# Optimization experiments

Measured on AMD Instinct MI355X. Metric: run time of the kernel, lower is better.

The kernel has to match this reference:

```python
import jax, jax.numpy as jnp
import numpy as np

B, S, IN, H = 16, 512, 512, 256
TAU_TRACE = 20.0
TAU_MEM = 20.0
DECAY_TRACE = float(np.exp(-1.0 / TAU_TRACE))  # exp_convolve decay
DECAY_MEM = float(np.exp(-1.0 / TAU_MEM))      # leaky-integrator dynamics decay
LR = 0.01                                       # plasticity learning rate
W_MAX = 1.0                                     # soft upper bound on fast weights


def setup_inputs() -> dict:
    key = jax.random.key(0)
    k1, k2 = jax.random.split(key)
    x = jax.random.normal(k1, (B, S, IN), dtype=jnp.float32)
    # xavier_uniform with gain=sqrt(2) on W of shape [2H, IN]
    lim = float(np.sqrt(2.0) * np.sqrt(6.0 / (2 * H + IN)))
    W = jax.random.uniform(k2, (2 * H, IN), dtype=jnp.float32, minval=-lim, maxval=lim)
    return {"x": x, "W": W}


def reference(x, W):
    # i = x @ W^T : [B, S, 2H], then split into key/value input currents
    i = jnp.einsum('bsi,hi->bsh', x, W)
    ik, iv = jnp.split(i, 2, axis=2)  # each [B, S, H]
    bsz = x.shape[0]
    h = W.shape[0] // 2

    def step(carry, inp):
        kv, vv, kt, vt, mem = carry
        ik_t, iv_t = inp  # [B, H] each
        # key dynamics (leaky integrator + tanh)
        kv = DECAY_MEM * kv + ik_t
        key = jnp.tanh(kv)
        # memory readout: 0.2 * (key.unsqueeze(1) * mem).sum(2) == 0.2 * mem @ key
        ikv = 0.2 * jnp.einsum('bij,bj->bi', mem, key)
        # value dynamics
        vv = DECAY_MEM * vv + iv_t + ikv
        val = jnp.tanh(vv)
        # exponential traces
        kt = DECAY_TRACE * kt + (1.0 - DECAY_TRACE) * key
        vt = DECAY_TRACE * vt + (1.0 - DECAY_TRACE) * val
        # soft-bounded Hebbian outer-product fast-weight update
        mem = mem + LR * (vt[:, :, None] * kt[:, None, :]) * (W_MAX - mem)
        return (kv, vv, kt, vt, mem), (key, val)

    z = jnp.zeros((bsz, h), x.dtype)
    mem0 = jnp.zeros((bsz, h, h), x.dtype)
    (_, _, _, _, mem), (keys, vals) = jax.lax.scan(
        step, (z, z, z, z, mem0),
        (jnp.swapaxes(ik, 0, 1), jnp.swapaxes(iv, 0, 1)))  # scan over time
    return mem, jnp.swapaxes(keys, 0, 1), jnp.swapaxes(vals, 0, 1)
```

## Files before the change

### kernel.cpp

```cpp
#include <hip/hip_runtime.h>

#define BB 16
#define SS 512
#define KIN 512
#define H 256

typedef float v2f __attribute__((ext_vector_type(2)));

constexpr float DECAY  = 0.951229424500714f;
constexpr float OMD    = 0.048770575499286f;
constexpr float DECAY8 = 0.670320046035639f;
constexpr float LR     = 0.01f;
constexpr float CLO    = 4.8770575499286e-4f;

__device__ __forceinline__ float fast_tanh(float x) {
    float e = __expf(2.f * x);
    return 1.f - __fdividef(2.f, e + 1.f);
}

__device__ __forceinline__ v2f pk_mul(v2f a, v2f b) {
    v2f d; asm("v_pk_mul_f32 %0, %1, %2" : "=v"(d) : "v"(a), "v"(b)); return d;
}
__device__ __forceinline__ v2f pk_fma(v2f a, v2f b, v2f c) {
    v2f d; asm("v_pk_fma_f32 %0, %1, %2, %3" : "=v"(d) : "v"(a), "v"(b), "v"(c)); return d;
}

__device__ __forceinline__ void allred32x2(float x, float y, float& rx, float& ry) {
    int t, u;
    t = __builtin_amdgcn_update_dpp(0, __float_as_int(x), 0x111, 0xf, 0xf, false);
    u = __builtin_amdgcn_update_dpp(0, __float_as_int(y), 0x111, 0xf, 0xf, false);
    x += __int_as_float(t); y += __int_as_float(u);
    t = __builtin_amdgcn_update_dpp(0, __float_as_int(x), 0x112, 0xf, 0xf, false);
    u = __builtin_amdgcn_update_dpp(0, __float_as_int(y), 0x112, 0xf, 0xf, false);
    x += __int_as_float(t); y += __int_as_float(u);
    t = __builtin_amdgcn_update_dpp(0, __float_as_int(x), 0x114, 0xf, 0xf, false);
    u = __builtin_amdgcn_update_dpp(0, __float_as_int(y), 0x114, 0xf, 0xf, false);
    x += __int_as_float(t); y += __int_as_float(u);
    t = __builtin_amdgcn_update_dpp(0, __float_as_int(x), 0x118, 0xf, 0xf, false);
    u = __builtin_amdgcn_update_dpp(0, __float_as_int(y), 0x118, 0xf, 0xf, false);
    x += __int_as_float(t); y += __int_as_float(u);
    t = __builtin_amdgcn_update_dpp(0, __float_as_int(x), 0x142, 0xa, 0xf, false);
    u = __builtin_amdgcn_update_dpp(0, __float_as_int(y), 0x142, 0xa, 0xf, false);
    x += __int_as_float(t); y += __int_as_float(u);
    rx = __int_as_float(__builtin_amdgcn_ds_swizzle(__float_as_int(x), 0x3E0));
    ry = __int_as_float(__builtin_amdgcn_ds_swizzle(__float_as_int(y), 0x3E0));
}

__global__ __launch_bounds__(256) void gemm_xwT(const float* __restrict__ X,
                                                const float* __restrict__ W,
                                                float* __restrict__ ik_out,
                                                float* __restrict__ iv_t) {
    __shared__ float As[2][16][132];
    __shared__ float Bs[2][16][68];
    const int m0 = blockIdx.y * 128;
    const int n0 = blockIdx.x * 64;
    const int tid = threadIdx.x;
    const int ra = tid >> 1;
    const int ca = (tid & 1) * 8;
    const int rb = tid >> 2;
    const int cb = (tid & 3) * 4;
    const int tx = tid & 15;
    const int ty = tid >> 4;

    const float* xp = &X[(size_t)(m0 + ra) * KIN + ca];
    const float* wp = &W[(size_t)(n0 + rb) * KIN + cb];

    float acc[8][4] = {};
    float4 a0 = *(const float4*)(xp);
    float4 a1 = *(const float4*)(xp + 4);
    float4 bv = *(const float4*)(wp);
    As[0][ca+0][ra] = a0.x; As[0][ca+1][ra] = a0.y; As[0][ca+2][ra] = a0.z; As[0][ca+3][ra] = a0.w;
    As[0][ca+4][ra] = a1.x; As[0][ca+5][ra] = a1.y; As[0][ca+6][ra] = a1.z; As[0][ca+7][ra] = a1.w;
    Bs[0][cb+0][rb] = bv.x; Bs[0][cb+1][rb] = bv.y; Bs[0][cb+2][rb] = bv.z; Bs[0][cb+3][rb] = bv.w;
    __syncthreads();

    int cur = 0;
    for (int c = 0; c < KIN / 16; ++c) {
        if (c + 1 < KIN / 16) {
            a0 = *(const float4*)(xp + (size_t)(c + 1) * 16);
            a1 = *(const float4*)(xp + (size_t)(c + 1) * 16 + 4);
            bv = *(const float4*)(wp + (size_t)(c + 1) * 16);
        }
#pragma unroll
        for (int kk = 0; kk < 16; ++kk) {
            float4 A0 = *(const float4*)&As[cur][kk][ty * 8];
            float4 A1 = *(const float4*)&As[cur][kk][ty * 8 + 4];
            float4 B  = *(const float4*)&Bs[cur][kk][tx * 4];
            float arr[8] = {A0.x, A0.y, A0.z, A0.w, A1.x, A1.y, A1.z, A1.w};
            float brr[4] = {B.x, B.y, B.z, B.w};
#pragma unroll
            for (int i = 0; i < 8; ++i)
#pragma unroll
                for (int j = 0; j < 4; ++j) acc[i][j] += arr[i] * brr[j];
        }
        if (c + 1 < KIN / 16) {
            const int nb = cur ^ 1;
            As[nb][ca+0][ra] = a0.x; As[nb][ca+1][ra] = a0.y;
            As[nb][ca+2][ra] = a0.z; As[nb][ca+3][ra] = a0.w;
            As[nb][ca+4][ra] = a1.x; As[nb][ca+5][ra] = a1.y;
            As[nb][ca+6][ra] = a1.z; As[nb][ca+7][ra] = a1.w;
            Bs[nb][cb+0][rb] = bv.x; Bs[nb][cb+1][rb] = bv.y;
            Bs[nb][cb+2][rb] = bv.z; Bs[nb][cb+3][rb] = bv.w;
            __syncthreads();
            cur = nb;
        }
    }

    if (n0 < 256) {
#pragma unroll
        for (int i = 0; i < 8; ++i) {
            float4 o = make_float4(acc[i][0], acc[i][1], acc[i][2], acc[i][3]);
            *(float4*)&ik_out[(size_t)(m0 + ty * 8 + i) * 256 + n0 + tx * 4] = o;
        }
    } else {
        const int b  = m0 >> 9;
        const int s0 = (m0 & 511) + ty * 8;
#pragma unroll
        for (int j = 0; j < 4; ++j) {
            float* dst = &iv_t[((size_t)b * H + (n0 - 256 + tx * 4 + j)) * SS + s0];
            *(float4*)(dst)     = make_float4(acc[0][j], acc[1][j], acc[2][j], acc[3][j]);
            *(float4*)(dst + 4) = make_float4(acc[4][j], acc[5][j], acc[6][j], acc[7][j]);
        }
    }
}


__global__ __launch_bounds__(256) void ks1_chunk(const float* __restrict__ ik,
                                                 float* __restrict__ E) {
    const int col = threadIdx.x;
    const int b   = blockIdx.x >> 6;
    const int ch  = blockIdx.x & 63;
    const float* p = ik + ((size_t)(b * SS + ch * 8)) * 256 + col;
    float rb[8];
#pragma unroll
    for (int j = 0; j < 8; ++j) rb[j] = p[(size_t)j * 256];
    float e = 0.f;
#pragma unroll
    for (int j = 0; j < 8; ++j) e = __builtin_fmaf(DECAY, e, rb[j]);
    E[((size_t)b * 64 + ch) * 256 + col] = e;
}

__global__ __launch_bounds__(64) void ks2_carry(const float* __restrict__ E,
                                                float* __restrict__ Sst) {
    const int idx = blockIdx.x * 64 + threadIdx.x;
    const int b   = idx >> 8;
    const int col = idx & 255;
    const float* Eb = E + (size_t)b * 64 * 256 + col;
    float* Sb = Sst + (size_t)b * 64 * 256 + col;
    float eb[64];
#pragma unroll
    for (int c = 0; c < 64; ++c) eb[c] = Eb[(size_t)c * 256];
    float carry = 0.f;
#pragma unroll
    for (int c = 0; c < 64; ++c) {
        Sb[(size_t)c * 256] = carry;
        carry = __builtin_fmaf(DECAY8, carry, eb[c]);
    }
}

__global__ __launch_bounds__(256) void ks3_emit(const float* __restrict__ ik,
                                                const float* __restrict__ Sst,
                                                float* __restrict__ keys) {
    const int col = threadIdx.x;
    const int b   = blockIdx.x >> 6;
    const int ch  = blockIdx.x & 63;
    const float* p = ik + ((size_t)(b * SS + ch * 8)) * 256 + col;
    float* ko = keys + ((size_t)(b * SS + ch * 8)) * H + col;
    float rb[8];
#pragma unroll
    for (int j = 0; j < 8; ++j) rb[j] = p[(size_t)j * 256];
    float kv = Sst[((size_t)b * 64 + ch) * 256 + col];
#pragma unroll
    for (int j = 0; j < 8; ++j) {
        kv = __builtin_fmaf(DECAY, kv, rb[j]);
        ko[(size_t)j * H] = fast_tanh(kv);
    }
}

__global__ __launch_bounds__(256, 2) void value_scan(const float* __restrict__ keys,
                                                     const float* __restrict__ iv_t,
                                                     float* __restrict__ mem_out,
                                                     float* __restrict__ vals) {
    const int tid  = threadIdx.x;
    const int wave = tid >> 6;
    const int lane = tid & 63;
    const int sub  = lane & 31;
    const int half = lane >> 5;
    const int b    = blockIdx.x & 15;
    const int rg   = blockIdx.x >> 4;
    const int row  = rg * 8 + wave * 2 + half;
    const int so   = sub * 8;

    const float* kp  = keys + (size_t)b * SS * H + so;
    const float* ivp = iv_t + ((size_t)b * H + row) * SS;
    float* vrow = vals + (size_t)b * SS * H + row;

    const v2f DEC2 = {DECAY, DECAY};

    v2f nm0 = {0.f,0.f}, nm1 = {0.f,0.f}, nm2 = {0.f,0.f}, nm3 = {0.f,0.f};
    v2f w0  = {0.f,0.f}, w1  = {0.f,0.f}, w2  = {0.f,0.f}, w3  = {0.f,0.f};
    v2f kt0 = {0.f,0.f}, kt1 = {0.f,0.f}, kt2 = {0.f,0.f}, kt3 = {0.f,0.f};
    float vv = 0.f, vt = 0.f, c = 0.f, ar = 0.f, br = 0.f, stash = 0.f;

    v2f kp0 = *(const v2f*)(kp + 0), kp1 = *(const v2f*)(kp + 2),
        kp2 = *(const v2f*)(kp + 4), kp3 = *(const v2f*)(kp + 6);
    v2f kR[4][4];
#pragma unroll
    for (int j = 0; j < 4; ++j)
#pragma unroll
        for (int q = 0; q < 4; ++q)
            kR[j][q] = *(const v2f*)(kp + (size_t)(1 + j) * H + q * 2);
    const float* kpF = kp + 5 * H;

    float4 iA0 = *(const float4*)(ivp + 0);
    float4 iA1 = *(const float4*)(ivp + 4);
    float4 iB0 = *(const float4*)(ivp + 8);
    float4 iB1 = *(const float4*)(ivp + 12);
    ivp += 16;

#define VS_STEP(J, RELK)                                                       \
    {                                                                          \
        v2f kc0 = kR[(J)&3][0], kc1 = kR[(J)&3][1],                            \
            kc2 = kR[(J)&3][2], kc3 = kR[(J)&3][3];                            \
        if (RELK) {                                                            \
            kR[(J)&3][0] = *(const v2f*)(kpF + ((J)&3) * H + 0);               \
            kR[(J)&3][1] = *(const v2f*)(kpF + ((J)&3) * H + 2);               \
            kR[(J)&3][2] = *(const v2f*)(kpF + ((J)&3) * H + 4);               \
            kR[(J)&3][3] = *(const v2f*)(kpF + ((J)&3) * H + 6);               \
        }                                                                      \
        v2f nc2 = {-c, -c};                                                    \
        nm0 = pk_fma(nc2, w0, nm0);                                            \
        nm1 = pk_fma(nc2, w1, nm1);                                            \
        nm2 = pk_fma(nc2, w2, nm2);                                            \
        nm3 = pk_fma(nc2, w3, nm3);                                            \
        kt0 = pk_fma(DEC2, kt0, kp0);                                          \
        kt1 = pk_fma(DEC2, kt1, kp1);                                          \
        kt2 = pk_fma(DEC2, kt2, kp2);                                          \
        kt3 = pk_fma(DEC2, kt3, kp3);                                          \
        w0 = pk_fma(kt0, nm0, kt0);                                            \
        w1 = pk_fma(kt1, nm1, kt1);                                            \
        w2 = pk_fma(kt2, nm2, kt2);                                            \
        w3 = pk_fma(kt3, nm3, kt3);                                            \
        v2f a2 = pk_mul(nm0, kc0);                                             \
        a2 = pk_fma(nm1, kc1, a2);                                             \
        a2 = pk_fma(nm2, kc2, a2);                                             \
        a2 = pk_fma(nm3, kc3, a2);                                             \
        v2f b2 = pk_mul(w0, kc0);                                              \
        b2 = pk_fma(w1, kc1, b2);                                              \
        b2 = pk_fma(w2, kc2, b2);                                              \
        b2 = pk_fma(w3, kc3, b2);                                              \
        float ra, rb2;                                                         \
        allred32x2(a2.x + a2.y, b2.x + b2.y, ra, rb2);                         \
        float arn = -0.2f * ra;                                                \
        float brn =  0.2f * rb2;                                               \
        kp0 = kc0; kp1 = kc1; kp2 = kc2; kp3 = kc3;                            \
        float vvt = __builtin_fmaf(DECAY, vv, ivs[J]) + ar;                    \
        vv = __builtin_fmaf(c, br, vvt);                                       \
        float valv = fast_tanh(vv);                                            \
        vt = __builtin_fmaf(DECAY, vt, OMD * valv);                            \
        if (sub == (J)) stash = valv;                                          \
        c = CLO * vt;                                                          \
        ar = arn; br = brn;                                                    \
        asm volatile("" ::: "memory");                                         \
    }

    for (int t0 = 0; t0 < SS - 16; t0 += 16) {
        float4 nA0 = *(const float4*)(ivp + 0);
        float4 nA1 = *(const float4*)(ivp + 4);
        float4 nB0 = *(const float4*)(ivp + 8);
        float4 nB1 = *(const float4*)(ivp + 12);
        ivp += 16;
        {
            float ivs[16] = {iA0.x, iA0.y, iA0.z, iA0.w,
                             iA1.x, iA1.y, iA1.z, iA1.w,
                             iB0.x, iB0.y, iB0.z, iB0.w,
                             iB1.x, iB1.y, iB1.z, iB1.w};
            VS_STEP(0, 1)  VS_STEP(1, 1)  VS_STEP(2, 1)  VS_STEP(3, 1)
            kpF += 4 * H;
            VS_STEP(4, 1)  VS_STEP(5, 1)  VS_STEP(6, 1)  VS_STEP(7, 1)
            kpF += 4 * H;
            VS_STEP(8, 1)  VS_STEP(9, 1)  VS_STEP(10, 1) VS_STEP(11, 1)
            kpF += 4 * H;
            VS_STEP(12, 1) VS_STEP(13, 1) VS_STEP(14, 1) VS_STEP(15, 1)
            kpF += 4 * H;
        }
        if (sub < 16) vrow[(size_t)sub * H] = stash;
        vrow += 16 * H;
        iA0 = nA0; iA1 = nA1; iB0 = nB0; iB1 = nB1;
    }
    {
        float ivs[16] = {iA0.x, iA0.y, iA0.z, iA0.w,
                         iA1.x, iA1.y, iA1.z, iA1.w,
                         iB0.x, iB0.y, iB0.z, iB0.w,
                         iB1.x, iB1.y, iB1.z, iB1.w};
        VS_STEP(0, 1)  VS_STEP(1, 1)  VS_STEP(2, 1)  VS_STEP(3, 1)
        kpF += 4 * H;
        VS_STEP(4, 1)  VS_STEP(5, 1)  VS_STEP(6, 1)  VS_STEP(7, 1)
        kpF += 4 * H;
        VS_STEP(8, 1)  VS_STEP(9, 1)  VS_STEP(10, 1) VS_STEP(11, 0)
        VS_STEP(12, 0) VS_STEP(13, 0) VS_STEP(14, 0) VS_STEP(15, 0)
        if (sub < 16) vrow[(size_t)sub * H] = stash;
    }
#undef VS_STEP

    {
        v2f ncf = {-c, -c};
        nm0 = pk_fma(ncf, w0, nm0);
        nm1 = pk_fma(ncf, w1, nm1);
        nm2 = pk_fma(ncf, w2, nm2);
        nm3 = pk_fma(ncf, w3, nm3);
    }
    float* mo = &mem_out[((size_t)b * H + row) * H + so];
    *(float4*)&mo[0] = make_float4(-nm0.x, -nm0.y, -nm1.x, -nm1.y);
    *(float4*)&mo[4] = make_float4(-nm2.x, -nm2.y, -nm3.x, -nm3.y);
}

extern "C" void kernel_launch(void* const* d_in, const int* in_sizes, int n_in,
                              void* d_out, int out_size, void* d_ws, size_t ws_size,
                              hipStream_t stream) {
    const float* x = (const float*)d_in[0];
    const float* W = (const float*)d_in[1];
    float* out = (float*)d_out;
    float* mem_out = out;
    float* keys = out + (size_t)BB * H * H;
    float* vals = keys + (size_t)BB * SS * H;
    float* ik   = (float*)d_ws;
    float* iv_t = ik + (size_t)BB * SS * 256;
    float* E    = vals;
    float* Sst  = vals + 262144;

    dim3 gb(8, 64);
    gemm_xwT<<<gb, 256, 0, stream>>>(x, W, ik, iv_t);
    ks1_chunk<<<1024, 256, 0, stream>>>(ik, E);
    ks2_carry<<<64, 64, 0, stream>>>(E, Sst);
    ks3_emit<<<1024, 256, 0, stream>>>(ik, Sst, keys);
    value_scan<<<512, 256, 0, stream>>>(keys, iv_t, mem_out, vals);
}
```

Before: 217.3 us.

## Fold chunk-carry scan into emit kernel and restructure key-trace update in value scan

Removes the separate ks2_carry launch. Each ks3_emit block now recomputes its own chunk carry by serially reading up to 63 chunk sums E. This trades one launch and a global round-trip for redundant loads and FMAs per block, which the L2 cache should absorb. In value_scan, the key-trace update is moved after the readout and consumes the current key directly, which drops the kp register copies and shortens the dependency chain.

```diff
diff --git a/kernel.cpp b/kernel.cpp
--- a/kernel.cpp
+++ b/kernel.cpp
@@ -140,36 +140,25 @@
     E[((size_t)b * 64 + ch) * 256 + col] = e;
 }
 
-__global__ __launch_bounds__(64) void ks2_carry(const float* __restrict__ E,
-                                                float* __restrict__ Sst) {
-    const int idx = blockIdx.x * 64 + threadIdx.x;
-    const int b   = idx >> 8;
-    const int col = idx & 255;
-    const float* Eb = E + (size_t)b * 64 * 256 + col;
-    float* Sb = Sst + (size_t)b * 64 * 256 + col;
-    float eb[64];
-#pragma unroll
-    for (int c = 0; c < 64; ++c) eb[c] = Eb[(size_t)c * 256];
-    float carry = 0.f;
-#pragma unroll
-    for (int c = 0; c < 64; ++c) {
-        Sb[(size_t)c * 256] = carry;
-        carry = __builtin_fmaf(DECAY8, carry, eb[c]);
-    }
-}
-
 __global__ __launch_bounds__(256) void ks3_emit(const float* __restrict__ ik,
-                                                const float* __restrict__ Sst,
+                                                const float* __restrict__ E,
                                                 float* __restrict__ keys) {
     const int col = threadIdx.x;
     const int b   = blockIdx.x >> 6;
     const int ch  = blockIdx.x & 63;
+    const float* Eb = E + (size_t)b * 64 * 256 + col;
+    float carry = 0.f;
+#pragma unroll
+    for (int c2 = 0; c2 < 63; ++c2) {
+        float ev = Eb[(size_t)c2 * 256];
+        if (c2 < ch) carry = __builtin_fmaf(DECAY8, carry, ev);
+    }
     const float* p = ik + ((size_t)(b * SS + ch * 8)) * 256 + col;
     float* ko = keys + ((size_t)(b * SS + ch * 8)) * H + col;
     float rb[8];
 #pragma unroll
     for (int j = 0; j < 8; ++j) rb[j] = p[(size_t)j * 256];
-    float kv = Sst[((size_t)b * 64 + ch) * 256 + col];
+    float kv = carry;
 #pragma unroll
     for (int j = 0; j < 8; ++j) {
         kv = __builtin_fmaf(DECAY, kv, rb[j]);
@@ -199,11 +188,10 @@
 
     v2f nm0 = {0.f,0.f}, nm1 = {0.f,0.f}, nm2 = {0.f,0.f}, nm3 = {0.f,0.f};
     v2f w0  = {0.f,0.f}, w1  = {0.f,0.f}, w2  = {0.f,0.f}, w3  = {0.f,0.f};
-    v2f kt0 = {0.f,0.f}, kt1 = {0.f,0.f}, kt2 = {0.f,0.f}, kt3 = {0.f,0.f};
     float vv = 0.f, vt = 0.f, c = 0.f, ar = 0.f, br = 0.f, stash = 0.f;
 
-    v2f kp0 = *(const v2f*)(kp + 0), kp1 = *(const v2f*)(kp + 2),
-        kp2 = *(const v2f*)(kp + 4), kp3 = *(const v2f*)(kp + 6);
+    v2f kt0 = *(const v2f*)(kp + 0), kt1 = *(const v2f*)(kp + 2),
+        kt2 = *(const v2f*)(kp + 4), kt3 = *(const v2f*)(kp + 6);
     v2f kR[4][4];
 #pragma unroll
     for (int j = 0; j < 4; ++j)
@@ -233,10 +221,6 @@
         nm1 = pk_fma(nc2, w1, nm1);                                            \
         nm2 = pk_fma(nc2, w2, nm2);                                            \
         nm3 = pk_fma(nc2, w3, nm3);                                            \
-        kt0 = pk_fma(DEC2, kt0, kp0);                                          \
-        kt1 = pk_fma(DEC2, kt1, kp1);                                          \
-        kt2 = pk_fma(DEC2, kt2, kp2);                                          \
-        kt3 = pk_fma(DEC2, kt3, kp3);                                          \
         w0 = pk_fma(kt0, nm0, kt0);                                            \
         w1 = pk_fma(kt1, nm1, kt1);                                            \
         w2 = pk_fma(kt2, nm2, kt2);                                            \
@@ -249,11 +233,14 @@
         b2 = pk_fma(w1, kc1, b2);                                              \
         b2 = pk_fma(w2, kc2, b2);                                              \
         b2 = pk_fma(w3, kc3, b2);                                              \
+        kt0 = pk_fma(DEC2, kt0, kc0);                                          \
+        kt1 = pk_fma(DEC2, kt1, kc1);                                          \
+        kt2 = pk_fma(DEC2, kt2, kc2);                                          \
+        kt3 = pk_fma(DEC2, kt3, kc3);                                          \
         float ra, rb2;                                                         \
         allred32x2(a2.x + a2.y, b2.x + b2.y, ra, rb2);                         \
         float arn = -0.2f * ra;                                                \
         float brn =  0.2f * rb2;                                               \
-        kp0 = kc0; kp1 = kc1; kp2 = kc2; kp3 = kc3;                            \
         float vvt = __builtin_fmaf(DECAY, vv, ivs[J]) + ar;                    \
         vv = __builtin_fmaf(c, br, vvt);                                       \
         float valv = fast_tanh(vv);                                            \
@@ -327,12 +314,10 @@
     float* ik   = (float*)d_ws;
     float* iv_t = ik + (size_t)BB * SS * 256;
     float* E    = vals;
-    float* Sst  = vals + 262144;
 
     dim3 gb(8, 64);
     gemm_xwT<<<gb, 256, 0, stream>>>(x, W, ik, iv_t);
     ks1_chunk<<<1024, 256, 0, stream>>>(ik, E);
-    ks2_carry<<<64, 64, 0, stream>>>(E, Sst);
-    ks3_emit<<<1024, 256, 0, stream>>>(ik, Sst, keys);
+    ks3_emit<<<1024, 256, 0, stream>>>(ik, E, keys);
     value_scan<<<512, 256, 0, stream>>>(keys, iv_t, mem_out, vals);
 }
```

Result: slower. 233.5 us (+7.5%).
